# Performance work log

Measured on AMD Instinct MI355X. Metric: run time of the kernel, lower is better.

Reference implementation:

```python
import jax, jax.numpy as jnp
import numpy as np
import math

B, N, C_IN = 4, 512, 32
K = 3            # Chebyshev order -> K+1 polynomial terms
H = 4            # attention heads
OUT_PER_HEAD = 64
ACT_OUT = OUT_PER_HEAD * H  # concat_heads=True


def _prelu(x, a):
    return jnp.where(x >= 0, x, a * x)


def setup_inputs() -> dict:
    key = jax.random.key(0)
    ks = jax.random.split(key, 10)
    stdv = 1.0 / math.sqrt(ACT_OUT)
    inp = {
        "X_real": jax.random.normal(ks[0], (B, N, C_IN), jnp.float32),
        "X_imag": jax.random.normal(ks[1], (B, N, C_IN), jnp.float32),
        "L_real": jax.random.normal(ks[2], (B, K + 1, N, N), jnp.float32),
        "L_imag": jax.random.normal(ks[3], (B, K + 1, N, N), jnp.float32),
        # Chebyshev complex weights, uniform(-stdv, stdv) as in torch init
        "weight_real": jax.random.uniform(ks[4], (K + 1, C_IN, ACT_OUT), jnp.float32, -stdv, stdv),
        "weight_imag": jax.random.uniform(ks[5], (K + 1, C_IN, ACT_OUT), jnp.float32, -stdv, stdv),
        # CVLinear(2*C_IN -> H) complex weight/bias
        "attn_w_real": jax.random.normal(ks[6], (2 * C_IN, H), jnp.float32) * 0.1,
        "attn_w_imag": jax.random.normal(ks[7], (2 * C_IN, H), jnp.float32) * 0.1,
        "attn_b_real": jnp.zeros((H,), jnp.float32),
        "attn_b_imag": jnp.zeros((H,), jnp.float32),
        # CPReLU slopes (PReLU applied to real/imag parts independently)
        "prelu_a_real": jnp.float32(0.25),
        "prelu_a_imag": jnp.float32(0.25),
        "bias_real": jnp.zeros((1, ACT_OUT), jnp.float32),
        "bias_imag": jnp.zeros((1, ACT_OUT), jnp.float32),
    }
    return inp


def reference(X_real, X_imag, L_real, L_imag, weight_real, weight_imag,
              attn_w_real, attn_w_imag, attn_b_real, attn_b_imag,
              prelu_a_real, prelu_a_imag, bias_real, bias_imag):
    C = X_real.shape[-1]
    K1 = weight_real.shape[0]
    # --- attention scores: complex linear on concat([X_i, X_j]) ---
    # split the 2C weight into the X_i half and the X_j half (same math,
    # avoids materializing the B*N*N*2C pairwise concat tensor)
    W1r, W2r = attn_w_real[:C], attn_w_real[C:]
    W1i, W2i = attn_w_imag[:C], attn_w_imag[C:]
    si_re = X_real @ W1r - X_imag @ W1i   # (B,N,H)
    si_im = X_real @ W1i + X_imag @ W1r
    sj_re = X_real @ W2r - X_imag @ W2i
    sj_im = X_real @ W2i + X_imag @ W2r
    # scores[b,i,j,h]
    sc_re = si_re[:, :, None, :] + sj_re[:, None, :, :] + attn_b_real
    sc_im = si_im[:, :, None, :] + sj_im[:, None, :, :] + attn_b_imag
    # CPReLU: PReLU on real/imag independently
    sc_re = _prelu(sc_re, prelu_a_real)
    sc_im = _prelu(sc_im, prelu_a_imag)
    # adjacency mask from |L_real| summed over the K+1 polynomial terms
    mask = (jnp.abs(L_real).sum(axis=1) > 1e-9)[..., None]  # (B,N,N,1)
    NEG = jnp.float32(-1e9)
    re_m = jnp.where(mask, sc_re, NEG)
    im_m = jnp.where(mask, sc_im, NEG)
    attn = jax.nn.softmax(re_m * re_m + im_m * im_m, axis=2)  # softmax over j, (B,N,N,H)
    # --- complex Chebyshev propagation: (L*attn) @ X, per k, per head ---
    lre_xr = jnp.einsum('bknj,bnjh,bjc->bknch', L_real, attn, X_real)
    lim_xi = jnp.einsum('bknj,bnjh,bjc->bknch', L_imag, attn, X_imag)
    lre_xi = jnp.einsum('bknj,bnjh,bjc->bknch', L_real, attn, X_imag)
    lim_xr = jnp.einsum('bknj,bnjh,bjc->bknch', L_imag, attn, X_real)
    LXr = lre_xr - lim_xi
    LXi = lre_xi + lim_xr
    # per-head complex weights: (K+1, C, P, H), out index = p*H + h
    Wr = weight_real.reshape(K1, C, OUT_PER_HEAD, H)
    Wi = weight_imag.reshape(K1, C, OUT_PER_HEAD, H)
    Yre = jnp.einsum('bknch,kcph->bnph', LXr, Wr) - jnp.einsum('bknch,kcph->bnph', LXi, Wi)
    Yim = jnp.einsum('bknch,kcph->bnph', LXr, Wi) + jnp.einsum('bknch,kcph->bnph', LXi, Wr)
    Bsz, Nn = X_real.shape[:2]
    out_re = Yre.reshape(Bsz, Nn, -1) + bias_real
    out_im = Yim.reshape(Bsz, Nn, -1) + bias_imag
    return (out_re, out_im)
```

## Files before the change

### kernel.cpp

```cpp
#include <hip/hip_runtime.h>
#include <hip/hip_bf16.h>

#define BB 4
#define NN 512
#define CC 32
#define KK 4
#define HH 4
#define AOUT 256

#define WS_SI_F   0
#define WS_SII_F  (BB*NN*HH)
#define WS_SJR_F  (2*BB*NN*HH)
#define WS_SJI_F  (3*BB*NN*HH)
#define XT_BASE   131072
#define LX_BASE   393216
#define BRE_BASE  4587520
#define BIM_BASE  4718592

typedef __attribute__((ext_vector_type(8))) short bf16x8;
typedef __attribute__((ext_vector_type(4))) float f32x4;

__device__ __forceinline__ ushort f2bfu(float f){
    union { __hip_bfloat16 h; ushort u; } cv;
    cv.h = __float2bfloat16(f);
    return cv.u;
}
__device__ __forceinline__ short f2bfs(float f){ return (short)f2bfu(f); }
__device__ __forceinline__ float bfu2f(unsigned int u){ return __uint_as_float(u << 16); }

__global__ __launch_bounds__(256) void prep_kernel(
    const float* __restrict__ Xr, const float* __restrict__ Xi,
    const float* __restrict__ AWr, const float* __restrict__ AWi,
    const float* __restrict__ Wr, const float* __restrict__ Wi,
    float* __restrict__ ws, char* __restrict__ wsB)
{
    const int blk = blockIdx.x;
    const int t = threadIdx.x;

    if (blk < 32) {
        const int row = blk*64 + (t >> 2);
        const int q = t & 3;
        const float* xr = Xr + (size_t)row*CC + q*8;
        const float* xi = Xi + (size_t)row*CC + q*8;
        float4 xr4[2], xi4[2];
        xr4[0] = *(const float4*)xr;  xr4[1] = *(const float4*)(xr + 4);
        xi4[0] = *(const float4*)xi;  xi4[1] = *(const float4*)(xi + 4);

        float sir[HH] = {0,0,0,0}, sii[HH] = {0,0,0,0};
        float sjr[HH] = {0,0,0,0}, sji[HH] = {0,0,0,0};
        #pragma unroll
        for (int e = 0; e < 8; ++e) {
            float xrc = ((const float*)&xr4[e>>2])[e & 3];
            float xic = ((const float*)&xi4[e>>2])[e & 3];
            int c = q*8 + e;
            float4 w1r = *(const float4*)(AWr + c*HH);
            float4 w1i = *(const float4*)(AWi + c*HH);
            float4 w2r = *(const float4*)(AWr + (CC + c)*HH);
            float4 w2i = *(const float4*)(AWi + (CC + c)*HH);
            #pragma unroll
            for (int h = 0; h < HH; ++h) {
                float r1 = ((const float*)&w1r)[h], i1 = ((const float*)&w1i)[h];
                float r2 = ((const float*)&w2r)[h], i2 = ((const float*)&w2i)[h];
                sir[h] = fmaf(xrc, r1, fmaf(-xic, i1, sir[h]));
                sii[h] = fmaf(xrc, i1, fmaf( xic, r1, sii[h]));
                sjr[h] = fmaf(xrc, r2, fmaf(-xic, i2, sjr[h]));
                sji[h] = fmaf(xrc, i2, fmaf( xic, r2, sji[h]));
            }
        }
        float A[HH], Bv[HH];
        #pragma unroll
        for (int h = 0; h < HH; ++h) {
            float sendA = (q & 1) ? sir[h] : sii[h];
            float keepA = (q & 1) ? sii[h] : sir[h];
            A[h] = keepA + __shfl_xor(sendA, 1);
            float sendB = (q & 1) ? sjr[h] : sji[h];
            float keepB = (q & 1) ? sji[h] : sjr[h];
            Bv[h] = keepB + __shfl_xor(sendB, 1);
        }
        float tot[HH];
        #pragma unroll
        for (int h = 0; h < HH; ++h) {
            float send = (q & 2) ? A[h] : Bv[h];
            float keep = (q & 2) ? Bv[h] : A[h];
            tot[h] = keep + __shfl_xor(send, 2);
        }
        float4 v = make_float4(tot[0], tot[1], tot[2], tot[3]);
        *(float4*)(ws + (size_t)q*(BB*NN*HH) + (size_t)row*HH) = v;
    } else if (blk < 64) {
        int bid = (blk - 32)*4 + (t >> 6);
        int part = bid >> 6, b = (bid >> 4) & 3, jb = bid & 15;
        const float* X = part ? Xi : Xr;
        int lane = t & 63;
        int c = lane & 31, jh = lane >> 5;

        unsigned int w[8];
        #pragma unroll
        for (int qq = 0; qq < 8; ++qq) {
            int ji = jh*16 + qq*2;
            float f0 = X[((size_t)b*NN + jb*32 + ji  )*CC + c];
            float f1 = X[((size_t)b*NN + jb*32 + ji+1)*CC + c];
            w[qq] = (unsigned int)f2bfu(f0) | ((unsigned int)f2bfu(f1) << 16);
        }
        char* tile = wsB + XT_BASE + (((size_t)(part*4 + b)*16 + jb) * 2048);
        uint4* dst = (uint4*)(tile + c*64 + jh*32);
        dst[0] = make_uint4(w[0], w[1], w[2], w[3]);
        dst[1] = make_uint4(w[4], w[5], w[6], w[7]);
    } else {
        int idx = (blk - 64)*256 + t;
        int l  = idx & 63;
        int s  = (idx >> 6) & 7;
        int Nt = (idx >> 9) & 3;
        int h  = idx >> 11;
        int p = Nt*16 + (l & 15), o = p*4 + h;
        int e8 = (l >> 4) * 8;
        unsigned int re_w[4], im_w[4];
        #pragma unroll
        for (int qq = 0; qq < 4; ++qq) {
            unsigned int rw = 0, iw = 0;
            #pragma unroll
            for (int half = 0; half < 2; ++half) {
                int kpos = s*32 + e8 + qq*2 + half;
                int ri = kpos >> 7, kk = (kpos >> 5) & 3, c = kpos & 31;
                float wr = Wr[(size_t)(kk*CC + c)*AOUT + o];
                float wi = Wi[(size_t)(kk*CC + c)*AOUT + o];
                unsigned int vre = f2bfu(ri ? -wi : wr);
                unsigned int vim = f2bfu(ri ?  wr : wi);
                rw |= vre << (16*half);
                iw |= vim << (16*half);
            }
            re_w[qq] = rw; im_w[qq] = iw;
        }
        size_t fo = ((size_t)((h*4 + Nt)*8 + s))*1024 + (size_t)l*16;
        *(uint4*)(wsB + BRE_BASE + fo) = make_uint4(re_w[0], re_w[1], re_w[2], re_w[3]);
        *(uint4*)(wsB + BIM_BASE + fo) = make_uint4(im_w[0], im_w[1], im_w[2], im_w[3]);
    }
}

__global__ __launch_bounds__(128, 4) void cheb_main_kernel(
    const float* __restrict__ Lr_g, const float* __restrict__ Li_g,
    const float* __restrict__ abr, const float* __restrict__ abi,
    const float* __restrict__ par, const float* __restrict__ pai,
    const float* __restrict__ ws, char* __restrict__ wsB)
{
    __shared__ ushort Lf[8][528];
    __shared__ float awf[HH][520];
    __shared__ float wredm[2][HH];
    __shared__ float wreds[2][HH];

    const int bn = blockIdx.x;
    const int b = bn >> 9;
    const int n = bn & (NN - 1);
    const int t = threadIdx.x;
    const int l = t & 63;
    const int w = t >> 6;
    const int jw = 4*t;

    const float4 si_r4 = *(const float4*)(ws + WS_SI_F  + bn*HH);
    const float4 si_i4 = *(const float4*)(ws + WS_SII_F + bn*HH);
    float4 sjr[4], sji[4];
    #pragma unroll
    for (int e = 0; e < 4; ++e) {
        sjr[e] = *(const float4*)(ws + WS_SJR_F + ((size_t)b*NN + jw + e)*HH);
        sji[e] = *(const float4*)(ws + WS_SJI_F + ((size_t)b*NN + jw + e)*HH);
    }
    const float a_r = par[0], a_i = pai[0];

    const char* xtR = wsB + XT_BASE + ((size_t)(0*4 + b)*16 + w*8)*2048;
    const char* xtI = wsB + XT_BASE + ((size_t)(4   + b)*16 + w*8)*2048;
    const int jg  = l >> 4;
    const int bofs = (l & 15)*64 + jg*16;

#define LB(s, BR0,BR1,BI0,BI1) do {                                           \
        BR0 = *(const bf16x8*)(xtR + (s)*2048 +        bofs);                 \
        BR1 = *(const bf16x8*)(xtR + (s)*2048 + 1024 + bofs);                 \
        BI0 = *(const bf16x8*)(xtI + (s)*2048 +        bofs);                 \
        BI1 = *(const bf16x8*)(xtI + (s)*2048 + 1024 + bofs);                 \
    } while (0)

    bf16x8 pR0,pR1,pI0,pI1, qR0,qR1,qI0,qI1, rR0,rR1,rI0,rI1;
    LB(0, pR0,pR1,pI0,pI1);
    LB(1, qR0,qR1,qI0,qI1);

    float am4[4] = {0.f,0.f,0.f,0.f};
    #pragma unroll
    for (int it = 0; it < 8; ++it) {
        const float* src = (it & 4) ? Li_g : Lr_g;
        size_t goff = (((size_t)b*KK + (it & 3))*NN + n)*NN + jw;
        float4 v = *(const float4*)(src + goff);
        if (it < 4) {
            am4[0] += fabsf(v.x); am4[1] += fabsf(v.y);
            am4[2] += fabsf(v.z); am4[3] += fabsf(v.w);
        }
        ushort4 u;
        u.x = f2bfu(v.x); u.y = f2bfu(v.y); u.z = f2bfu(v.z); u.w = f2bfu(v.w);
        *(ushort4*)&Lf[it][jw] = u;
    }

    float sir[HH], sii[HH];
    #pragma unroll
    for (int h = 0; h < HH; ++h) {
        sir[h] = ((const float*)&si_r4)[h] + abr[h];
        sii[h] = ((const float*)&si_i4)[h] + abi[h];
    }
    float v[4][HH];
    float pmax[HH] = {-INFINITY, -INFINITY, -INFINITY, -INFINITY};
    #pragma unroll
    for (int e = 0; e < 4; ++e) {
        bool msk = am4[e] > 1e-9f;
        const float* sjrp = (const float*)&sjr[e];
        const float* sjip = (const float*)&sji[e];
        #pragma unroll
        for (int h = 0; h < HH; ++h) {
            float sr = sir[h] + sjrp[h];
            sr = sr >= 0.f ? sr : a_r * sr;
            float sv = sii[h] + sjip[h];
            sv = sv >= 0.f ? sv : a_i * sv;
            float val;
            if (msk) val = sr*sr + sv*sv;
            else { const float NEG = -1e9f; val = NEG*NEG + NEG*NEG; }
            v[e][h] = val;
            pmax[h] = fmaxf(pmax[h], val);
        }
    }
    #pragma unroll
    for (int h = 0; h < HH; ++h) {
        #pragma unroll
        for (int off = 32; off > 0; off >>= 1)
            pmax[h] = fmaxf(pmax[h], __shfl_xor(pmax[h], off));
    }
    if (l == 0) { wredm[w][0]=pmax[0]; wredm[w][1]=pmax[1]; wredm[w][2]=pmax[2]; wredm[w][3]=pmax[3]; }
    __syncthreads();

    float hm[HH];
    #pragma unroll
    for (int h = 0; h < HH; ++h) hm[h] = fmaxf(wredm[0][h], wredm[1][h]);

    float psum[HH];
    #pragma unroll
    for (int h = 0; h < HH; ++h) {
        float4 ev;
        ev.x = __expf(v[0][h] - hm[h]);
        ev.y = __expf(v[1][h] - hm[h]);
        ev.z = __expf(v[2][h] - hm[h]);
        ev.w = __expf(v[3][h] - hm[h]);
        *(float4*)&awf[h][jw] = ev;
        psum[h] = (ev.x + ev.y) + (ev.z + ev.w);
    }
    #pragma unroll
    for (int h = 0; h < HH; ++h) {
        #pragma unroll
        for (int off = 32; off > 0; off >>= 1)
            psum[h] += __shfl_xor(psum[h], off);
    }
    if (l == 0) { wreds[w][0]=psum[0]; wreds[w][1]=psum[1]; wreds[w][2]=psum[2]; wreds[w][3]=psum[3]; }
    __syncthreads();

    float inv[HH];
    #pragma unroll
    for (int h = 0; h < HH; ++h) inv[h] = 1.0f / (wreds[0][h] + wreds[1][h]);

    const int r_a = l & 15;
    const int k_a = r_a >> 2, h_a = r_a & 3;

    f32x4 acc[8];
    #pragma unroll
    for (int a = 0; a < 8; ++a) acc[a] = (f32x4){0.f,0.f,0.f,0.f};

#define COMP(s, BR0,BR1,BI0,BI1) do {                                         \
        const int j0_ = w*256 + (s)*32 + jg*8;                                \
        bf16x8 LR8 = *(const bf16x8*)&Lf[k_a][j0_];                           \
        bf16x8 LI8 = *(const bf16x8*)&Lf[4 + k_a][j0_];                       \
        float aww_[8];                                                        \
        *(float4*)&aww_[0] = *(const float4*)&awf[h_a][j0_];                  \
        *(float4*)&aww_[4] = *(const float4*)&awf[h_a][j0_ + 4];              \
        bf16x8 Ar_, Ai_;                                                      \
        _Pragma("unroll")                                                     \
        for (int e_ = 0; e_ < 8; ++e_) {                                      \
            Ar_[e_] = f2bfs(bfu2f((ushort)LR8[e_]) * aww_[e_]);               \
            Ai_[e_] = f2bfs(bfu2f((ushort)LI8[e_]) * aww_[e_]);               \
        }                                                                     \
        acc[0] = __builtin_amdgcn_mfma_f32_16x16x32_bf16(Ar_, BR0, acc[0],0,0,0); \
        acc[1] = __builtin_amdgcn_mfma_f32_16x16x32_bf16(Ar_, BR1, acc[1],0,0,0); \
        acc[2] = __builtin_amdgcn_mfma_f32_16x16x32_bf16(Ai_, BI0, acc[2],0,0,0); \
        acc[3] = __builtin_amdgcn_mfma_f32_16x16x32_bf16(Ai_, BI1, acc[3],0,0,0); \
        acc[4] = __builtin_amdgcn_mfma_f32_16x16x32_bf16(Ar_, BI0, acc[4],0,0,0); \
        acc[5] = __builtin_amdgcn_mfma_f32_16x16x32_bf16(Ar_, BI1, acc[5],0,0,0); \
        acc[6] = __builtin_amdgcn_mfma_f32_16x16x32_bf16(Ai_, BR0, acc[6],0,0,0); \
        acc[7] = __builtin_amdgcn_mfma_f32_16x16x32_bf16(Ai_, BR1, acc[7],0,0,0); \
    } while (0)

    LB(2, rR0,rR1,rI0,rI1);  COMP(0, pR0,pR1,pI0,pI1);
    LB(3, pR0,pR1,pI0,pI1);  COMP(1, qR0,qR1,qI0,qI1);
    LB(4, qR0,qR1,qI0,qI1);  COMP(2, rR0,rR1,rI0,rI1);
    LB(5, rR0,rR1,rI0,rI1);  COMP(3, pR0,pR1,pI0,pI1);
    LB(6, pR0,pR1,pI0,pI1);  COMP(4, qR0,qR1,qI0,qI1);
    LB(7, qR0,qR1,qI0,qI1);  COMP(5, rR0,rR1,rI0,rI1);
    COMP(6, pR0,pR1,pI0,pI1);
    COMP(7, qR0,qR1,qI0,qI1);
#undef LB
#undef COMP

    __syncthreads();

    float* pbuf = &awf[0][0];
    if (w == 1) {
        #pragma unroll
        for (int ae = 0; ae < 4; ++ae)
            #pragma unroll
            for (int r = 0; r < 4; ++r)
                pbuf[(ae*4 + r)*64 + l] = acc[2*ae][r];
    } else {
        #pragma unroll
        for (int ao = 0; ao < 4; ++ao)
            #pragma unroll
            for (int r = 0; r < 4; ++r)
                pbuf[1024 + (ao*4 + r)*64 + l] = acc[2*ao + 1][r];
    }
    __syncthreads();

    const int kk = l >> 4, lc = l & 15;
    char* lxp = wsB + LX_BASE + (size_t)bn*2048;
    if (w == 0) {
        #pragma unroll
        for (int ae = 0; ae < 4; ++ae)
            #pragma unroll
            for (int r = 0; r < 4; ++r)
                acc[2*ae][r] += pbuf[(ae*4 + r)*64 + l];
        #pragma unroll
        for (int r = 0; r < 4; ++r) {
            float iv = inv[r];
            float vr = (acc[0][r] - acc[2][r]) * iv;
            float vi = (acc[4][r] + acc[6][r]) * iv;
            *(ushort*)(lxp + r*512 +       kk*64 + lc*2) = f2bfu(vr);
            *(ushort*)(lxp + r*512 + 256 + kk*64 + lc*2) = f2bfu(vi);
        }
    } else {
        #pragma unroll
        for (int ao = 0; ao < 4; ++ao)
            #pragma unroll
            for (int r = 0; r < 4; ++r)
                acc[2*ao + 1][r] += pbuf[1024 + (ao*4 + r)*64 + l];
        const int c = 16 + lc;
        #pragma unroll
        for (int r = 0; r < 4; ++r) {
            float iv = inv[r];
            float vr = (acc[1][r] - acc[3][r]) * iv;
            float vi = (acc[5][r] + acc[7][r]) * iv;
            *(ushort*)(lxp + r*512 +       kk*64 + c*2) = f2bfu(vr);
            *(ushort*)(lxp + r*512 + 256 + kk*64 + c*2) = f2bfu(vi);
        }
    }
}

__global__ __launch_bounds__(256) void out_gemm_kernel(
    const char* __restrict__ wsB,
    const float* __restrict__ bsr, const float* __restrict__ bsi,
    float* __restrict__ out)
{
    const int Mtile = blockIdx.x >> 2;
    const int Nt    = blockIdx.x & 3;
    const int t = threadIdx.x, l = t & 63, h = t >> 6;

    const char* abase = wsB + LX_BASE + ((size_t)(Mtile*16 + (l & 15)))*2048
                        + h*512 + (l >> 4)*16;
    f32x4 are = (f32x4){0.f,0.f,0.f,0.f};
    f32x4 aim = (f32x4){0.f,0.f,0.f,0.f};
    const size_t fbase = ((size_t)((h*4 + Nt)*8))*1024 + (size_t)l*16;
    const char* bre = wsB + BRE_BASE + fbase;
    const char* bim = wsB + BIM_BASE + fbase;
    #pragma unroll
    for (int s = 0; s < 8; ++s) {
        bf16x8 Af = *(const bf16x8*)(abase + s*64);
        bf16x8 Br = *(const bf16x8*)(bre + s*1024);
        bf16x8 Bi = *(const bf16x8*)(bim + s*1024);
        are = __builtin_amdgcn_mfma_f32_16x16x32_bf16(Af, Br, are, 0, 0, 0);
        aim = __builtin_amdgcn_mfma_f32_16x16x32_bf16(Af, Bi, aim, 0, 0, 0);
    }
    const int p = Nt*16 + (l & 15), o = p*4 + h;
    const float vbr = bsr[o], vbi = bsi[o];
    #pragma unroll
    for (int r = 0; r < 4; ++r) {
        int bn = Mtile*16 + (l >> 4)*4 + r;
        out[(size_t)bn*AOUT + o] = are[r] + vbr;
        out[(size_t)BB*NN*AOUT + (size_t)bn*AOUT + o] = aim[r] + vbi;
    }
}

extern "C" void kernel_launch(void* const* d_in, const int* in_sizes, int n_in,
                              void* d_out, int out_size, void* d_ws, size_t ws_size,
                              hipStream_t stream)
{
    const float* Xr  = (const float*)d_in[0];
    const float* Xi  = (const float*)d_in[1];
    const float* Lr  = (const float*)d_in[2];
    const float* Li  = (const float*)d_in[3];
    const float* Wr  = (const float*)d_in[4];
    const float* Wi  = (const float*)d_in[5];
    const float* AWr = (const float*)d_in[6];
    const float* AWi = (const float*)d_in[7];
    const float* abr = (const float*)d_in[8];
    const float* abi = (const float*)d_in[9];
    const float* par = (const float*)d_in[10];
    const float* pai = (const float*)d_in[11];
    const float* bsr = (const float*)d_in[12];
    const float* bsi = (const float*)d_in[13];
    float* ws  = (float*)d_ws;
    char*  wsB = (char*)d_ws;
    float* out = (float*)d_out;

    hipLaunchKernelGGL(prep_kernel, dim3(96), dim3(256), 0, stream,
                       Xr, Xi, AWr, AWi, Wr, Wi, ws, wsB);
    hipLaunchKernelGGL(cheb_main_kernel, dim3(BB*NN), dim3(128), 0, stream,
                       Lr, Li, abr, abi, par, pai, ws, wsB);
    hipLaunchKernelGGL(out_gemm_kernel, dim3(512), dim3(256), 0, stream,
                       wsB, bsr, bsi, out);
}
```

Measured before the change: 32.84 us.

## Use single-wave blocks in cheb_main, dropping cross-wave reductions and partial sums

The per-row kernel moves from two wavefronts to one 64-thread wavefront. Each thread now covers 8 columns, and the whole j-range MFMA loop runs in a single wave, so the shared-memory partial-accumulator merge, the cross-wave max/sum reductions and most __syncthreads disappear. Attention weights are stored in LDS as bf16 instead of fp32, which halves that footprint and the LDS read traffic. The trade-off is more registers per thread, fewer threads per block to hide the latency of the global L loads, and a little extra rounding of the softmax weights.

```diff
diff --git a/kernel.cpp b/kernel.cpp
--- a/kernel.cpp
+++ b/kernel.cpp
@@ -27,6 +27,9 @@
 }
 __device__ __forceinline__ short f2bfs(float f){ return (short)f2bfu(f); }
 __device__ __forceinline__ float bfu2f(unsigned int u){ return __uint_as_float(u << 16); }
+__device__ __forceinline__ unsigned int pk2(float lo, float hi){
+    return (unsigned int)f2bfu(lo) | ((unsigned int)f2bfu(hi) << 16);
+}
 
 __global__ __launch_bounds__(256) void prep_kernel(
     const float* __restrict__ Xr, const float* __restrict__ Xi,
@@ -136,39 +139,123 @@
     }
 }
 
-__global__ __launch_bounds__(128, 4) void cheb_main_kernel(
+__global__ __launch_bounds__(64) void cheb_main_kernel(
     const float* __restrict__ Lr_g, const float* __restrict__ Li_g,
     const float* __restrict__ abr, const float* __restrict__ abi,
     const float* __restrict__ par, const float* __restrict__ pai,
     const float* __restrict__ ws, char* __restrict__ wsB)
 {
-    __shared__ ushort Lf[8][528];
-    __shared__ float awf[HH][520];
-    __shared__ float wredm[2][HH];
-    __shared__ float wreds[2][HH];
+    __shared__ ushort Lf[8][544];
+    __shared__ ushort awB[HH][544];
 
     const int bn = blockIdx.x;
     const int b = bn >> 9;
     const int n = bn & (NN - 1);
     const int t = threadIdx.x;
-    const int l = t & 63;
-    const int w = t >> 6;
-    const int jw = 4*t;
-
-    const float4 si_r4 = *(const float4*)(ws + WS_SI_F  + bn*HH);
-    const float4 si_i4 = *(const float4*)(ws + WS_SII_F + bn*HH);
-    float4 sjr[4], sji[4];
-    #pragma unroll
-    for (int e = 0; e < 4; ++e) {
+    const int jw = 8*t;
+
+    float4 va[8], vb[8];
+    #pragma unroll
+    for (int it = 0; it < 8; ++it) {
+        const float* src = (it & 4) ? Li_g : Lr_g;
+        size_t goff = (((size_t)b*KK + (it & 3))*NN + n)*NN + jw;
+        va[it] = *(const float4*)(src + goff);
+        vb[it] = *(const float4*)(src + goff + 4);
+    }
+    float4 sjr[8], sji[8];
+    #pragma unroll
+    for (int e = 0; e < 8; ++e) {
         sjr[e] = *(const float4*)(ws + WS_SJR_F + ((size_t)b*NN + jw + e)*HH);
         sji[e] = *(const float4*)(ws + WS_SJI_F + ((size_t)b*NN + jw + e)*HH);
     }
+    const float4 si_r4 = *(const float4*)(ws + WS_SI_F  + (size_t)bn*HH);
+    const float4 si_i4 = *(const float4*)(ws + WS_SII_F + (size_t)bn*HH);
     const float a_r = par[0], a_i = pai[0];
 
-    const char* xtR = wsB + XT_BASE + ((size_t)(0*4 + b)*16 + w*8)*2048;
-    const char* xtI = wsB + XT_BASE + ((size_t)(4   + b)*16 + w*8)*2048;
-    const int jg  = l >> 4;
-    const int bofs = (l & 15)*64 + jg*16;
+    float am8[8] = {0.f,0.f,0.f,0.f,0.f,0.f,0.f,0.f};
+    #pragma unroll
+    for (int it = 0; it < 8; ++it) {
+        if (it < 4) {
+            am8[0] += fabsf(va[it].x); am8[1] += fabsf(va[it].y);
+            am8[2] += fabsf(va[it].z); am8[3] += fabsf(va[it].w);
+            am8[4] += fabsf(vb[it].x); am8[5] += fabsf(vb[it].y);
+            am8[6] += fabsf(vb[it].z); am8[7] += fabsf(vb[it].w);
+        }
+        uint4 W;
+        W.x = pk2(va[it].x, va[it].y);
+        W.y = pk2(va[it].z, va[it].w);
+        W.z = pk2(vb[it].x, vb[it].y);
+        W.w = pk2(vb[it].z, vb[it].w);
+        *(uint4*)&Lf[it][jw] = W;
+    }
+
+    float sir[HH], sii[HH];
+    #pragma unroll
+    for (int h = 0; h < HH; ++h) {
+        sir[h] = ((const float*)&si_r4)[h] + abr[h];
+        sii[h] = ((const float*)&si_i4)[h] + abi[h];
+    }
+    const float NEG = -1e9f;
+    const float MASKED = NEG*NEG + NEG*NEG;
+
+    float sc[8][HH];
+    float pm[HH] = {-INFINITY, -INFINITY, -INFINITY, -INFINITY};
+    #pragma unroll
+    for (int e = 0; e < 8; ++e) {
+        bool msk = am8[e] > 1e-9f;
+        const float* sjrp = (const float*)&sjr[e];
+        const float* sjip = (const float*)&sji[e];
+        #pragma unroll
+        for (int h = 0; h < HH; ++h) {
+            float sr = sir[h] + sjrp[h];
+            sr = sr >= 0.f ? sr : a_r * sr;
+            float sv = sii[h] + sjip[h];
+            sv = sv >= 0.f ? sv : a_i * sv;
+            float val = msk ? (sr*sr + sv*sv) : MASKED;
+            sc[e][h] = val;
+            pm[h] = fmaxf(pm[h], val);
+        }
+    }
+    #pragma unroll
+    for (int h = 0; h < HH; ++h) {
+        #pragma unroll
+        for (int off = 32; off > 0; off >>= 1)
+            pm[h] = fmaxf(pm[h], __shfl_xor(pm[h], off));
+    }
+    float ps[HH];
+    #pragma unroll
+    for (int h = 0; h < HH; ++h) {
+        float ev[8];
+        #pragma unroll
+        for (int e = 0; e < 8; ++e) ev[e] = __expf(sc[e][h] - pm[h]);
+        uint4 W;
+        W.x = pk2(ev[0], ev[1]);
+        W.y = pk2(ev[2], ev[3]);
+        W.z = pk2(ev[4], ev[5]);
+        W.w = pk2(ev[6], ev[7]);
+        *(uint4*)&awB[h][jw] = W;
+        ps[h] = ((ev[0]+ev[1]) + (ev[2]+ev[3])) + ((ev[4]+ev[5]) + (ev[6]+ev[7]));
+        #pragma unroll
+        for (int off = 32; off > 0; off >>= 1)
+            ps[h] += __shfl_xor(ps[h], off);
+    }
+    float inv[HH];
+    #pragma unroll
+    for (int h = 0; h < HH; ++h) inv[h] = 1.0f / ps[h];
+
+    __syncthreads();
+
+    const int r_a = t & 15;
+    const int jg  = t >> 4;
+    const int k_a = r_a >> 2, h_a = r_a & 3;
+
+    const char* xtR = wsB + XT_BASE + ((size_t)(0*4 + b)*16)*2048;
+    const char* xtI = wsB + XT_BASE + ((size_t)(4   + b)*16)*2048;
+    const int bofs = (t & 15)*64 + jg*16;
+
+    f32x4 acc[8];
+    #pragma unroll
+    for (int a = 0; a < 8; ++a) acc[a] = (f32x4){0.f,0.f,0.f,0.f};
 
 #define LB(s, BR0,BR1,BI0,BI1) do {                                           \
         BR0 = *(const bf16x8*)(xtR + (s)*2048 +        bofs);                 \
@@ -177,107 +264,17 @@
         BI1 = *(const bf16x8*)(xtI + (s)*2048 + 1024 + bofs);                 \
     } while (0)
 
-    bf16x8 pR0,pR1,pI0,pI1, qR0,qR1,qI0,qI1, rR0,rR1,rI0,rI1;
-    LB(0, pR0,pR1,pI0,pI1);
-    LB(1, qR0,qR1,qI0,qI1);
-
-    float am4[4] = {0.f,0.f,0.f,0.f};
-    #pragma unroll
-    for (int it = 0; it < 8; ++it) {
-        const float* src = (it & 4) ? Li_g : Lr_g;
-        size_t goff = (((size_t)b*KK + (it & 3))*NN + n)*NN + jw;
-        float4 v = *(const float4*)(src + goff);
-        if (it < 4) {
-            am4[0] += fabsf(v.x); am4[1] += fabsf(v.y);
-            am4[2] += fabsf(v.z); am4[3] += fabsf(v.w);
-        }
-        ushort4 u;
-        u.x = f2bfu(v.x); u.y = f2bfu(v.y); u.z = f2bfu(v.z); u.w = f2bfu(v.w);
-        *(ushort4*)&Lf[it][jw] = u;
-    }
-
-    float sir[HH], sii[HH];
-    #pragma unroll
-    for (int h = 0; h < HH; ++h) {
-        sir[h] = ((const float*)&si_r4)[h] + abr[h];
-        sii[h] = ((const float*)&si_i4)[h] + abi[h];
-    }
-    float v[4][HH];
-    float pmax[HH] = {-INFINITY, -INFINITY, -INFINITY, -INFINITY};
-    #pragma unroll
-    for (int e = 0; e < 4; ++e) {
-        bool msk = am4[e] > 1e-9f;
-        const float* sjrp = (const float*)&sjr[e];
-        const float* sjip = (const float*)&sji[e];
-        #pragma unroll
-        for (int h = 0; h < HH; ++h) {
-            float sr = sir[h] + sjrp[h];
-            sr = sr >= 0.f ? sr : a_r * sr;
-            float sv = sii[h] + sjip[h];
-            sv = sv >= 0.f ? sv : a_i * sv;
-            float val;
-            if (msk) val = sr*sr + sv*sv;
-            else { const float NEG = -1e9f; val = NEG*NEG + NEG*NEG; }
-            v[e][h] = val;
-            pmax[h] = fmaxf(pmax[h], val);
-        }
-    }
-    #pragma unroll
-    for (int h = 0; h < HH; ++h) {
-        #pragma unroll
-        for (int off = 32; off > 0; off >>= 1)
-            pmax[h] = fmaxf(pmax[h], __shfl_xor(pmax[h], off));
-    }
-    if (l == 0) { wredm[w][0]=pmax[0]; wredm[w][1]=pmax[1]; wredm[w][2]=pmax[2]; wredm[w][3]=pmax[3]; }
-    __syncthreads();
-
-    float hm[HH];
-    #pragma unroll
-    for (int h = 0; h < HH; ++h) hm[h] = fmaxf(wredm[0][h], wredm[1][h]);
-
-    float psum[HH];
-    #pragma unroll
-    for (int h = 0; h < HH; ++h) {
-        float4 ev;
-        ev.x = __expf(v[0][h] - hm[h]);
-        ev.y = __expf(v[1][h] - hm[h]);
-        ev.z = __expf(v[2][h] - hm[h]);
-        ev.w = __expf(v[3][h] - hm[h]);
-        *(float4*)&awf[h][jw] = ev;
-        psum[h] = (ev.x + ev.y) + (ev.z + ev.w);
-    }
-    #pragma unroll
-    for (int h = 0; h < HH; ++h) {
-        #pragma unroll
-        for (int off = 32; off > 0; off >>= 1)
-            psum[h] += __shfl_xor(psum[h], off);
-    }
-    if (l == 0) { wreds[w][0]=psum[0]; wreds[w][1]=psum[1]; wreds[w][2]=psum[2]; wreds[w][3]=psum[3]; }
-    __syncthreads();
-
-    float inv[HH];
-    #pragma unroll
-    for (int h = 0; h < HH; ++h) inv[h] = 1.0f / (wreds[0][h] + wreds[1][h]);
-
-    const int r_a = l & 15;
-    const int k_a = r_a >> 2, h_a = r_a & 3;
-
-    f32x4 acc[8];
-    #pragma unroll
-    for (int a = 0; a < 8; ++a) acc[a] = (f32x4){0.f,0.f,0.f,0.f};
-
 #define COMP(s, BR0,BR1,BI0,BI1) do {                                         \
-        const int j0_ = w*256 + (s)*32 + jg*8;                                \
+        const int j0_ = (s)*32 + jg*8;                                        \
         bf16x8 LR8 = *(const bf16x8*)&Lf[k_a][j0_];                           \
         bf16x8 LI8 = *(const bf16x8*)&Lf[4 + k_a][j0_];                       \
-        float aww_[8];                                                        \
-        *(float4*)&aww_[0] = *(const float4*)&awf[h_a][j0_];                  \
-        *(float4*)&aww_[4] = *(const float4*)&awf[h_a][j0_ + 4];              \
+        bf16x8 AW8 = *(const bf16x8*)&awB[h_a][j0_];                          \
         bf16x8 Ar_, Ai_;                                                      \
         _Pragma("unroll")                                                     \
         for (int e_ = 0; e_ < 8; ++e_) {                                      \
-            Ar_[e_] = f2bfs(bfu2f((ushort)LR8[e_]) * aww_[e_]);               \
-            Ai_[e_] = f2bfs(bfu2f((ushort)LI8[e_]) * aww_[e_]);               \
+            float awv = bfu2f((ushort)AW8[e_]);                               \
+            Ar_[e_] = f2bfs(bfu2f((ushort)LR8[e_]) * awv);                    \
+            Ai_[e_] = f2bfs(bfu2f((ushort)LI8[e_]) * awv);                    \
         }                                                                     \
         acc[0] = __builtin_amdgcn_mfma_f32_16x16x32_bf16(Ar_, BR0, acc[0],0,0,0); \
         acc[1] = __builtin_amdgcn_mfma_f32_16x16x32_bf16(Ar_, BR1, acc[1],0,0,0); \
@@ -289,63 +286,33 @@
         acc[7] = __builtin_amdgcn_mfma_f32_16x16x32_bf16(Ai_, BR1, acc[7],0,0,0); \
     } while (0)
 
-    LB(2, rR0,rR1,rI0,rI1);  COMP(0, pR0,pR1,pI0,pI1);
-    LB(3, pR0,pR1,pI0,pI1);  COMP(1, qR0,qR1,qI0,qI1);
-    LB(4, qR0,qR1,qI0,qI1);  COMP(2, rR0,rR1,rI0,rI1);
-    LB(5, rR0,rR1,rI0,rI1);  COMP(3, pR0,pR1,pI0,pI1);
-    LB(6, pR0,pR1,pI0,pI1);  COMP(4, qR0,qR1,qI0,qI1);
-    LB(7, qR0,qR1,qI0,qI1);  COMP(5, rR0,rR1,rI0,rI1);
-    COMP(6, pR0,pR1,pI0,pI1);
-    COMP(7, qR0,qR1,qI0,qI1);
+    {
+        bf16x8 pR0,pR1,pI0,pI1, qR0,qR1,qI0,qI1;
+        LB(0, pR0,pR1,pI0,pI1);
+        LB(1, qR0,qR1,qI0,qI1);
+        #pragma unroll
+        for (int s = 0; s < 14; s += 2) {
+            COMP(s,   pR0,pR1,pI0,pI1);
+            LB(s+2,   pR0,pR1,pI0,pI1);
+            COMP(s+1, qR0,qR1,qI0,qI1);
+            LB(s+3,   qR0,qR1,qI0,qI1);
+        }
+        COMP(14, pR0,pR1,pI0,pI1);
+        COMP(15, qR0,qR1,qI0,qI1);
+    }
 #undef LB
 #undef COMP
 
-    __syncthreads();
-
-    float* pbuf = &awf[0][0];
-    if (w == 1) {
-        #pragma unroll
-        for (int ae = 0; ae < 4; ++ae)
-            #pragma unroll
-            for (int r = 0; r < 4; ++r)
-                pbuf[(ae*4 + r)*64 + l] = acc[2*ae][r];
-    } else {
-        #pragma unroll
-        for (int ao = 0; ao < 4; ++ao)
-            #pragma unroll
-            for (int r = 0; r < 4; ++r)
-                pbuf[1024 + (ao*4 + r)*64 + l] = acc[2*ao + 1][r];
-    }
-    __syncthreads();
-
-    const int kk = l >> 4, lc = l & 15;
+    const int kk = t >> 4, lc = t & 15;
     char* lxp = wsB + LX_BASE + (size_t)bn*2048;
-    if (w == 0) {
-        #pragma unroll
-        for (int ae = 0; ae < 4; ++ae)
-            #pragma unroll
-            for (int r = 0; r < 4; ++r)
-                acc[2*ae][r] += pbuf[(ae*4 + r)*64 + l];
+    #pragma unroll
+    for (int ct = 0; ct < 2; ++ct) {
+        const int c = ct*16 + lc;
         #pragma unroll
         for (int r = 0; r < 4; ++r) {
             float iv = inv[r];
-            float vr = (acc[0][r] - acc[2][r]) * iv;
-            float vi = (acc[4][r] + acc[6][r]) * iv;
-            *(ushort*)(lxp + r*512 +       kk*64 + lc*2) = f2bfu(vr);
-            *(ushort*)(lxp + r*512 + 256 + kk*64 + lc*2) = f2bfu(vi);
-        }
-    } else {
-        #pragma unroll
-        for (int ao = 0; ao < 4; ++ao)
-            #pragma unroll
-            for (int r = 0; r < 4; ++r)
-                acc[2*ao + 1][r] += pbuf[1024 + (ao*4 + r)*64 + l];
-        const int c = 16 + lc;
-        #pragma unroll
-        for (int r = 0; r < 4; ++r) {
-            float iv = inv[r];
-            float vr = (acc[1][r] - acc[3][r]) * iv;
-            float vi = (acc[5][r] + acc[7][r]) * iv;
+            float vr = (acc[0+ct][r] - acc[2+ct][r]) * iv;
+            float vi = (acc[4+ct][r] + acc[6+ct][r]) * iv;
             *(ushort*)(lxp + r*512 +       kk*64 + c*2) = f2bfu(vr);
             *(ushort*)(lxp + r*512 + 256 + kk*64 + c*2) = f2bfu(vi);
         }
@@ -410,7 +377,7 @@
 
     hipLaunchKernelGGL(prep_kernel, dim3(96), dim3(256), 0, stream,
                        Xr, Xi, AWr, AWi, Wr, Wi, ws, wsB);
-    hipLaunchKernelGGL(cheb_main_kernel, dim3(BB*NN), dim3(128), 0, stream,
+    hipLaunchKernelGGL(cheb_main_kernel, dim3(BB*NN), dim3(64), 0, stream,
                        Lr, Li, abr, abi, par, pai, ws, wsB);
     hipLaunchKernelGGL(out_gemm_kernel, dim3(512), dim3(256), 0, stream,
                        wsB, bsr, bsi, out);
```

Result: slower. 36.37 us (+10.8%).
